# Kernel optimization log

Measured on AMD Instinct MI355X. Metric: run time of the kernel, lower is better.

## Reference

```python
import jax, jax.numpy as jnp
import numpy as np

TOTAL_NODES = 131072
IN_FEA = 512
RANK = 256
NUM_GRAPHS = 1024


def setup_inputs() -> dict:
    key = jax.random.key(0)
    kx, kw, kb, ks = jax.random.split(key, 4)
    x = jax.random.normal(kx, (TOTAL_NODES, IN_FEA), dtype=jnp.float32)
    W = jax.random.normal(kw, (RANK, IN_FEA), dtype=jnp.float32) * (1.0 / np.sqrt(IN_FEA))
    b = jax.random.normal(kb, (RANK,), dtype=jnp.float32)
    segment_ids = jnp.sort(jax.random.randint(ks, (TOTAL_NODES,), 0, NUM_GRAPHS, dtype=jnp.int32))
    return {"x": x, "W": W, "b": b, "segment_ids": segment_ids, "num_segments": NUM_GRAPHS}


def reference(x, W, b, segment_ids, num_segments):
    # per-node projection + tanh: [total_nodes, rank]
    t = jnp.tanh(x @ W.T + b)
    # multiplicative reduction over the nodes of each graph -> [num_graphs, rank]
    return jax.ops.segment_prod(t, segment_ids, num_segments=num_segments)
```

## Files before the change

### kernel.cpp

```cpp
#include <hip/hip_runtime.h>
#include <hip/hip_bf16.h>
#include <stdint.h>

#define M_TOTAL 131072
#define K_DIM   512
#define N_RANK  256
#define NSEG    1024
#define KC      64
#define NKC     (K_DIM / KC)
#define BM      128
#define NBLK    (M_TOTAL / BM)
#define NB64    (M_TOTAL / 64)

typedef __attribute__((ext_vector_type(8))) short bf16x8;
typedef __attribute__((ext_vector_type(4))) float f32x4;

#define BAR() do { \
    asm volatile("s_waitcnt lgkmcnt(0)" ::: "memory"); \
    __builtin_amdgcn_s_barrier(); \
} while (0)

__device__ inline short f2b(float f) {
    __hip_bfloat16 h = __float2bfloat16(f);
    return __builtin_bit_cast(short, h);
}

__device__ inline float fast_tanh(float z) {
    float e = __expf(2.0f * fabsf(z));
    return copysignf(1.0f - 2.0f / (e + 1.0f), z);
}

__global__ void prep_kernel(const float* __restrict__ W,
                            __hip_bfloat16* __restrict__ Wb,
                            float* __restrict__ out) {
    int i = blockIdx.x * 256 + threadIdx.x;
    out[i] = 1.0f;
    if (i < N_RANK * K_DIM) Wb[i] = __float2bfloat16(W[i]);
}

__launch_bounds__(512, 4)
__global__ void fused_kernel(const float* __restrict__ x,
                             const __hip_bfloat16* __restrict__ Wb,
                             const float* __restrict__ bias,
                             const int* __restrict__ seg,
                             float* __restrict__ out,
                             float* __restrict__ partial) {
    const int tid  = threadIdx.x;
    const int wave = tid >> 6;
    const int lane = tid & 63;
    const int l16  = lane & 15;
    const int g    = lane >> 4;
    const int bid  = blockIdx.x;
    const int m0   = bid * BM;
    const int n0   = wave * 32;

    __shared__ alignas(16) char smem[65536];

    const int drow = lane >> 4;
    const int dc16 = lane & 15;

    f32x4 acc[8][2] = {};

    #define DMA_CHUNK(kc_, buf_)                                              \
        do {                                                                  \
            _Pragma("unroll")                                                 \
            for (int t = 0; t < 4; ++t) {                                     \
                const int r7   = (4 * t + drow) & 7;                          \
                const int cf   = ((dc16 ^ r7) << 2);       \
                const float* gsrc = x + (size_t)(m0 + 16 * wave + 4 * t + drow) * K_DIM \
                                      + (kc_) * KC + cf;                      \
                uint32_t* ldst = reinterpret_cast<uint32_t*>(                 \
                    smem + (buf_) * 32768 + (wave * 4 + t) * 1024);           \
                __builtin_amdgcn_global_load_lds(                             \
                    reinterpret_cast<const uint32_t*>(gsrc), ldst, 16, 0, 0); \
            }                                                                 \
        } while (0)

    DMA_CHUNK(0, 0);

    #pragma unroll
    for (int kc = 0; kc < NKC; ++kc) {
        BAR();

        bf16x8 bfr[2][2];
        #pragma unroll
        for (int s = 0; s < 2; ++s)
            #pragma unroll
            for (int j = 0; j < 2; ++j)
                bfr[s][j] = *reinterpret_cast<const bf16x8*>(
                    Wb + (size_t)(n0 + j * 16 + l16) * K_DIM + kc * KC + s * 32 + g * 8);
        __builtin_amdgcn_sched_barrier(0);

        if (kc + 1 < NKC) DMA_CHUNK(kc + 1, (kc + 1) & 1);
        __builtin_amdgcn_sched_barrier(0);

        asm volatile("s_waitcnt vmcnt(4)" ::: "memory");
        BAR();

        const int bufb = (kc & 1) * 32768;
        #pragma unroll
        for (int s = 0; s < 2; ++s) {
            #pragma unroll
            for (int i = 0; i < 8; ++i) {
                const int row = i * 16 + l16;
                const int X   = (l16 & 7) << 4;
                const int c0  = s * 128 + g * 32;
                f32x4 lo = *reinterpret_cast<const f32x4*>(smem + bufb + row * 256 + (c0 ^ X));
                f32x4 hi = *reinterpret_cast<const f32x4*>(smem + bufb + row * 256 + ((c0 + 16) ^ X));
                bf16x8 av;
                av[0] = f2b(lo[0]); av[1] = f2b(lo[1]);
                av[2] = f2b(lo[2]); av[3] = f2b(lo[3]);
                av[4] = f2b(hi[0]); av[5] = f2b(hi[1]);
                av[6] = f2b(hi[2]); av[7] = f2b(hi[3]);
                #pragma unroll
                for (int j = 0; j < 2; ++j)
                    acc[i][j] = __builtin_amdgcn_mfma_f32_16x16x32_bf16(
                        av, bfr[s][j], acc[i][j], 0, 0, 0);
            }
        }
    }
    #undef DMA_CHUNK

    #pragma unroll
    for (int j = 0; j < 2; ++j) {
        const float bj = bias[n0 + j * 16 + l16];
        #pragma unroll
        for (int i = 0; i < 8; ++i)
            #pragma unroll
            for (int r = 0; r < 4; ++r)
                acc[i][j][r] = fast_tanh(acc[i][j][r] + bj);
    }

    #pragma unroll
    for (int h = 0; h < 2; ++h) {
        const int vb     = bid * 2 + h;
        const int myseg  = seg[m0 + h * 64 + lane];
        const int prevsg = (lane == 0) ? (myseg ^ 1) : seg[m0 + h * 64 + lane - 1];
        uint64_t m = __ballot(myseg != prevsg);

        while (m) {
            const int start = (int)__builtin_ctzll(m);
            m &= m - 1;
            const int end = m ? (int)__builtin_ctzll(m) : 64;
            const int s   = __shfl(myseg, start);

            float p[2] = {1.0f, 1.0f};
            #pragma unroll
            for (int i2 = 0; i2 < 4; ++i2)
                #pragma unroll
                for (int r = 0; r < 4; ++r) {
                    const int row = i2 * 16 + g * 4 + r;
                    const bool in = (row >= start) && (row < end);
                    #pragma unroll
                    for (int j = 0; j < 2; ++j)
                        p[j] *= in ? acc[h * 4 + i2][j][r] : 1.0f;
                }
            #pragma unroll
            for (int j = 0; j < 2; ++j) {
                p[j] *= __shfl_xor(p[j], 16);
                p[j] *= __shfl_xor(p[j], 32);
            }
            if (g == 0) {
                #pragma unroll
                for (int j = 0; j < 2; ++j) {
                    const int col = n0 + j * 16 + l16;
                    if (start == 0)
                        partial[(size_t)(vb * 2 + 0) * N_RANK + col] = p[j];
                    else if (end == 64)
                        partial[(size_t)(vb * 2 + 1) * N_RANK + col] = p[j];
                    else
                        out[(size_t)s * N_RANK + col] = p[j];
                }
            }
        }
    }
}

__global__ void pass2_kernel(const int* __restrict__ seg,
                             const float* __restrict__ partial,
                             float* __restrict__ out) {
    const int b   = blockIdx.x;
    const int col = threadIdx.x;
    const int sF    = seg[b * 64];
    const int sL    = seg[b * 64 + 63];
    const int prevL = (b == 0) ? -1 : seg[b * 64 - 1];

    if (prevL < sF) {
        float p = partial[(size_t)(b * 2 + 0) * N_RANK + col];
        for (int b2 = b + 1; b2 < NB64 && seg[b2 * 64] == sF; ++b2)
            p *= partial[(size_t)(b2 * 2 + 0) * N_RANK + col];
        out[(size_t)sF * N_RANK + col] = p;
    }
    if (sL != sF) {
        float p = partial[(size_t)(b * 2 + 1) * N_RANK + col];
        for (int b2 = b + 1; b2 < NB64 && seg[b2 * 64] == sL; ++b2)
            p *= partial[(size_t)(b2 * 2 + 0) * N_RANK + col];
        out[(size_t)sL * N_RANK + col] = p;
    }
}

extern "C" void kernel_launch(void* const* d_in, const int* in_sizes, int n_in,
                              void* d_out, int out_size, void* d_ws, size_t ws_size,
                              hipStream_t stream) {
    const float* x   = (const float*)d_in[0];
    const float* W   = (const float*)d_in[1];
    const float* b   = (const float*)d_in[2];
    const int*   seg = (const int*)d_in[3];
    float*       out = (float*)d_out;
    __hip_bfloat16* Wb = (__hip_bfloat16*)d_ws;
    float* partial = (float*)((char*)d_ws + (1 << 20));

    prep_kernel<<<(NSEG * N_RANK) / 256, 256, 0, stream>>>(W, Wb, out);
    fused_kernel<<<NBLK, 512, 0, stream>>>(x, Wb, b, seg, out, partial);
    pass2_kernel<<<NB64, 256, 0, stream>>>(seg, partial, out);
}
```

Before: 95.51 us.

## Stage x through registers and store bf16 to LDS once per block

Replaces the direct global-to-LDS fp32 DMA with register-staged loads. Each tile is converted to bf16 once on the way into LDS, instead of every wave converting the same fp32 data on every read. This halves LDS size and LDS read traffic and removes redundant conversions, so occupancy can rise. The cost is register pressure from holding the next tile across the MFMA loop, plus a full vmcnt(0) wait before each write. The loop also drops the second barrier, which may create a race between writing the next buffer and other waves still reading it.

```diff
diff --git a/kernel.cpp b/kernel.cpp
--- a/kernel.cpp
+++ b/kernel.cpp
@@ -54,29 +54,38 @@
     const int m0   = bid * BM;
     const int n0   = wave * 32;
 
-    __shared__ alignas(16) char smem[65536];
-
-    const int drow = lane >> 4;
-    const int dc16 = lane & 15;
+    __shared__ alignas(16) char smem[32768];
+
+    const int srow = tid >> 4;
+    const int sc16 = tid & 15;
 
     f32x4 acc[8][2] = {};
-
-    #define DMA_CHUNK(kc_, buf_)                                              \
+    f32x4 sg[4];
+
+    #define STAGE_LOAD(kc_)                                                   \
         do {                                                                  \
             _Pragma("unroll")                                                 \
-            for (int t = 0; t < 4; ++t) {                                     \
-                const int r7   = (4 * t + drow) & 7;                          \
-                const int cf   = ((dc16 ^ r7) << 2);       \
-                const float* gsrc = x + (size_t)(m0 + 16 * wave + 4 * t + drow) * K_DIM \
-                                      + (kc_) * KC + cf;                      \
-                uint32_t* ldst = reinterpret_cast<uint32_t*>(                 \
-                    smem + (buf_) * 32768 + (wave * 4 + t) * 1024);           \
-                __builtin_amdgcn_global_load_lds(                             \
-                    reinterpret_cast<const uint32_t*>(gsrc), ldst, 16, 0, 0); \
+            for (int it = 0; it < 4; ++it)                                    \
+                sg[it] = *reinterpret_cast<const f32x4*>(                     \
+                    x + (size_t)(m0 + it * 32 + srow) * K_DIM + (kc_) * KC + sc16 * 4); \
+        } while (0)
+
+    #define STAGE_WRITE(buf_)                                                 \
+        do {                                                                  \
+            _Pragma("unroll")                                                 \
+            for (int it = 0; it < 4; ++it) {                                  \
+                const int row = it * 32 + srow;                               \
+                short4 p;                                                     \
+                p.x = f2b(sg[it][0]); p.y = f2b(sg[it][1]);                   \
+                p.z = f2b(sg[it][2]); p.w = f2b(sg[it][3]);                   \
+                *reinterpret_cast<short4*>(smem + (buf_) * 16384 + row * 128  \
+                    + ((sc16 * 8) ^ ((row & 7) << 4))) = p;                   \
             }                                                                 \
         } while (0)
 
-    DMA_CHUNK(0, 0);
+    STAGE_LOAD(0);
+    asm volatile("s_waitcnt vmcnt(0)" ::: "memory");
+    STAGE_WRITE(0);
 
     #pragma unroll
     for (int kc = 0; kc < NKC; ++kc) {
@@ -91,35 +100,31 @@
                     Wb + (size_t)(n0 + j * 16 + l16) * K_DIM + kc * KC + s * 32 + g * 8);
         __builtin_amdgcn_sched_barrier(0);
 
-        if (kc + 1 < NKC) DMA_CHUNK(kc + 1, (kc + 1) & 1);
+        if (kc + 1 < NKC) STAGE_LOAD(kc + 1);
         __builtin_amdgcn_sched_barrier(0);
 
-        asm volatile("s_waitcnt vmcnt(4)" ::: "memory");
-        BAR();
-
-        const int bufb = (kc & 1) * 32768;
+        const int bufb = (kc & 1) * 16384;
         #pragma unroll
         for (int s = 0; s < 2; ++s) {
             #pragma unroll
             for (int i = 0; i < 8; ++i) {
                 const int row = i * 16 + l16;
-                const int X   = (l16 & 7) << 4;
-                const int c0  = s * 128 + g * 32;
-                f32x4 lo = *reinterpret_cast<const f32x4*>(smem + bufb + row * 256 + (c0 ^ X));
-                f32x4 hi = *reinterpret_cast<const f32x4*>(smem + bufb + row * 256 + ((c0 + 16) ^ X));
-                bf16x8 av;
-                av[0] = f2b(lo[0]); av[1] = f2b(lo[1]);
-                av[2] = f2b(lo[2]); av[3] = f2b(lo[3]);
-                av[4] = f2b(hi[0]); av[5] = f2b(hi[1]);
-                av[6] = f2b(hi[2]); av[7] = f2b(hi[3]);
+                bf16x8 av = *reinterpret_cast<const bf16x8*>(
+                    smem + bufb + row * 128 + ((s * 64 + g * 16) ^ ((row & 7) << 4)));
                 #pragma unroll
                 for (int j = 0; j < 2; ++j)
                     acc[i][j] = __builtin_amdgcn_mfma_f32_16x16x32_bf16(
                         av, bfr[s][j], acc[i][j], 0, 0, 0);
             }
         }
-    }
-    #undef DMA_CHUNK
+
+        if (kc + 1 < NKC) {
+            asm volatile("s_waitcnt vmcnt(0)" ::: "memory");
+            STAGE_WRITE((kc + 1) & 1);
+        }
+    }
+    #undef STAGE_LOAD
+    #undef STAGE_WRITE
 
     #pragma unroll
     for (int j = 0; j < 2; ++j) {
```

Result: faster. 81.39 us (-14.8%).
